# Performance work log

Measured on AMD Instinct MI355X. Metric: run time of the kernel, lower is better.

## Reference

```python
import jax, jax.numpy as jnp
import numpy as np

S_INIT, S_FINAL = 512, 1024
LAYER_DIM, NEXT_DIM, DIM = 512, 512, 1024
BATCH = 32768


def setup_inputs() -> dict:
    rng = np.random.default_rng(0)
    # eigenvector block (trainable 'base') and its 0/1 mask
    base = np.zeros((DIM, DIM), dtype=np.float32)
    base[S_INIT:S_FINAL, S_INIT - LAYER_DIM:S_INIT] = rng.uniform(
        -0.2, 0.2, (NEXT_DIM, LAYER_DIM)).astype(np.float32)
    base_mask = np.zeros((DIM, DIM), dtype=np.float32)
    base_mask[S_INIT:S_FINAL, S_INIT - LAYER_DIM:S_INIT] = 1.0
    eye = np.eye(DIM, dtype=np.float32)
    # eigenvalue diagonal block; NOTE: trainable_diag_mask holds the *random values*
    # (not 0/1), exactly as in the original TF code.
    masks = np.zeros((DIM, DIM), dtype=np.float32)
    masks[S_INIT:S_FINAL, S_INIT:S_FINAL] = np.diag(
        rng.uniform(-1.8, 1.8, NEXT_DIM).astype(np.float32))
    untrainable_diag = eye - masks
    trainable_diag = masks.copy()
    trainable_diag_mask = masks.copy()
    # column masks selecting pass-through rows vs. activated block rows
    mask1 = np.ones((DIM, 1), dtype=np.float32)
    mask1[S_INIT:S_FINAL] = 0.0
    mask2 = np.zeros((DIM, 1), dtype=np.float32)
    mask2[S_INIT:S_FINAL] = 1.0

    key = jax.random.key(0)
    data = jax.random.normal(key, (BATCH, DIM), dtype=jnp.float32)
    return {
        "data": data,
        "base": jnp.asarray(base),
        "base_mask": jnp.asarray(base_mask),
        "eye": jnp.asarray(eye),
        "trainable_diag": jnp.asarray(trainable_diag),
        "trainable_diag_mask": jnp.asarray(trainable_diag_mask),
        "untrainable_diag": jnp.asarray(untrainable_diag),
        "mask1": jnp.asarray(mask1),
        "mask2": jnp.asarray(mask2),
    }


def reference(data, base, base_mask, eye, trainable_diag, trainable_diag_mask,
              untrainable_diag, mask1, mask2):
    # layer = masked base + I ; diag = masked trainable diag + (I - fixed diag)
    layer = base * base_mask + eye                                  # [D, D]
    diag = trainable_diag * trainable_diag_mask + untrainable_diag  # [D, D]
    x = jnp.matmul(2.0 * eye - layer, data.T)                       # [D, B]
    x = jnp.matmul(diag, x)                                         # [D, B]
    x = jnp.matmul(layer, x)                                        # [D, B]
    temp = jax.nn.relu(x)  # relu is elementwise; transpose pair cancels
    x = x * mask1 + temp * mask2                                    # [D, B]
    return x.T                                                      # [B, D]
```

## Files before the change

### kernel.cpp

```cpp
#include <hip/hip_runtime.h>


typedef float f32x4 __attribute__((ext_vector_type(4)));
typedef int   i32x4 __attribute__((ext_vector_type(4)));

#define DIMW   1024
#define HALFD  512
#define BM     64
#define LDAP   520
#define NITER  16

__device__ __forceinline__ unsigned short f2bf(float x) {
    union { float f; unsigned int i; } c;
    c.f = x;
    unsigned int r = c.i + 0x7FFFu + ((c.i >> 16) & 1u);
    return (unsigned short)(r >> 16);
}
__device__ __forceinline__ unsigned int pack2(float a, float b) {
    return (unsigned int)f2bf(a) | ((unsigned int)f2bf(b) << 16);
}

__device__ __forceinline__ void mfma_16x16x32_bf16(f32x4& d, const i32x4& a, const i32x4& b) {
    asm volatile("v_mfma_f32_16x16x32_bf16 %0, %1, %2, %0"
                 : "+v"(d)
                 : "v"(a), "v"(b));
}
__device__ __forceinline__ void acc_fence(f32x4& d) {
    asm volatile("s_nop 7\n\ts_nop 7" : "+v"(d));
}

__global__ __launch_bounds__(512, 4) void spectral_kernel(
    const float* __restrict__ data,
    const float* __restrict__ wsrc,
    const float* __restrict__ td,
    const float* __restrict__ tdm,
    const float* __restrict__ ud,
    float* __restrict__ out)
{
    __shared__ unsigned short As[BM * LDAP];

    const int tid    = (int)threadIdx.x;
    const int lane   = tid & 63;
    const int wn     = tid >> 6;
    const int lane16 = lane & 15;
    const int quad   = lane >> 4;
    const int rowBase = (int)blockIdx.x * BM;

    #pragma unroll
    for (int p = 0; p < 16; ++p) {
        int c  = p * 512 + tid;
        int r  = c >> 7;
        int cc = c & 127;
        size_t off = (size_t)(rowBase + r) * DIMW + cc * 4;
        float4 v = *(const float4*)(data + off);
        *(float4*)(out + off) = v;
        uint2 uu;
        uu.x = pack2(v.x, v.y);
        uu.y = pack2(v.z, v.w);
        *(uint2*)(As + r * LDAP + cc * 4) = uu;
    }

    i32x4 b0[4], b1[4];

    auto LDW = [&](int it, i32x4 (&b)[4]) {
        #pragma unroll
        for (int ni = 0; ni < 4; ++ni) {
            int col = wn * 64 + ni * 16 + lane16;
            const float* p = wsrc + (size_t)(HALFD + col) * DIMW + it * 32 + quad * 8;
            float4 f0 = *(const float4*)p;
            float4 f1 = *(const float4*)(p + 4);
            i32x4 t;
            t[0] = (int)pack2(f0.x, f0.y);  t[1] = (int)pack2(f0.z, f0.w);
            t[2] = (int)pack2(f1.x, f1.y);  t[3] = (int)pack2(f1.z, f1.w);
            b[ni] = t;
        }
    };

    LDW(0, b0);
    LDW(1, b1);
    __syncthreads();

    f32x4 acc[4][4];
    #pragma unroll
    for (int mi = 0; mi < 4; ++mi)
        #pragma unroll
        for (int ni = 0; ni < 4; ++ni)
            acc[mi][ni] = (f32x4){0.f, 0.f, 0.f, 0.f};

    auto STEP = [&](int it, i32x4 (&b)[4]) {
        i32x4 a[4];
        #pragma unroll
        for (int mi = 0; mi < 4; ++mi)
            a[mi] = *(const i32x4*)(As + (mi * 16 + lane16) * LDAP + it * 32 + quad * 8);
        #pragma unroll
        for (int mi = 0; mi < 4; ++mi)
            #pragma unroll
            for (int ni = 0; ni < 4; ++ni)
                mfma_16x16x32_bf16(acc[mi][ni], a[mi], b[ni]);
    };

    #pragma unroll
    for (int it = 0; it < NITER; it += 2) {
        STEP(it, b0);
        if (it + 2 < NITER) LDW(it + 2, b0);
        STEP(it + 1, b1);
        if (it + 3 < NITER) LDW(it + 3, b1);
    }

    #pragma unroll
    for (int mi = 0; mi < 4; ++mi)
        #pragma unroll
        for (int ni = 0; ni < 4; ++ni)
            acc_fence(acc[mi][ni]);

    #pragma unroll
    for (int ni = 0; ni < 4; ++ni) {
        const int nloc = wn * 64 + ni * 16 + lane16;
        const int j  = HALFD + nloc;
        const size_t fi = (size_t)j * DIMW + j;
        const float dv = td[fi] * tdm[fi] + ud[fi];
        #pragma unroll
        for (int mi = 0; mi < 4; ++mi) {
            const int mBase = rowBase + mi * 16 + quad * 4;
            #pragma unroll
            for (int r = 0; r < 4; ++r) {
                const size_t gi = (size_t)(mBase + r) * DIMW + j;
                const float u1 = data[gi];
                const float v  = dv * u1 + (1.0f - dv) * acc[mi][ni][r];
                out[gi] = fmaxf(v, 0.0f);
            }
        }
    }
}

extern "C" void kernel_launch(void* const* d_in, const int* in_sizes, int n_in,
                              void* d_out, int out_size, void* d_ws, size_t ws_size,
                              hipStream_t stream) {
    const float* data = (const float*)d_in[0];
    const float* base = (const float*)d_in[1];
    const float* td   = (const float*)d_in[4];
    const float* tdm  = (const float*)d_in[5];
    const float* ud   = (const float*)d_in[6];
    float* out = (float*)d_out;

    dim3 block(512, 1, 1);
    dim3 grid(32768 / BM, 1, 1);
    spectral_kernel<<<grid, block, 0, stream>>>(data, base, td, tdm, ud, out);
}
```

Before: 367.4 us.

## Split passthrough copy into dedicated blocks and vectorize epilogue via swapped MFMA operands

Adds 256 extra blocks that only copy the pass-through half of the output (the first 512 columns), so GEMM blocks no longer write it. GEMM blocks now load only the left half for the bf16 A tile, batch eight loads before their stores, and cache the diagonal values in shared memory. MFMA operands are swapped so each lane owns four consecutive columns, which lets the epilogue read data and write out with float4 accesses instead of scalar strided ones. The costs are a larger grid with mixed block roles and the copy blocks' tail behaviour.

Result: faster. 346.8 us (-5.6%).

```diff
diff --git a/kernel.cpp b/kernel.cpp
--- a/kernel.cpp
+++ b/kernel.cpp
@@ -9,6 +9,7 @@
 #define BM     64
 #define LDAP   520
 #define NITER  16
+#define NCOPY  256
 
 __device__ __forceinline__ unsigned short f2bf(float x) {
     union { float f; unsigned int i; } c;
@@ -37,27 +38,68 @@
     const float* __restrict__ ud,
     float* __restrict__ out)
 {
+    const int tid = (int)threadIdx.x;
+
+    if ((int)blockIdx.x < NCOPY) {
+        const int rowBase = (int)blockIdx.x * 128;
+        const float4* src = (const float4*)data;
+        float4*       dst = (float4*)out;
+        #pragma unroll
+        for (int h = 0; h < 4; ++h) {
+            float4 v[8];
+            #pragma unroll
+            for (int p = 0; p < 8; ++p) {
+                int c  = (h * 8 + p) * 512 + tid;
+                int r  = c >> 7;
+                int cc = c & 127;
+                v[p] = src[(size_t)(rowBase + r) * (DIMW / 4) + cc];
+            }
+            #pragma unroll
+            for (int p = 0; p < 8; ++p) {
+                int c  = (h * 8 + p) * 512 + tid;
+                int r  = c >> 7;
+                int cc = c & 127;
+                dst[(size_t)(rowBase + r) * (DIMW / 4) + cc] = v[p];
+            }
+        }
+        return;
+    }
+
     __shared__ unsigned short As[BM * LDAP];
+    __shared__ float dsh[HALFD];
 
-    const int tid    = (int)threadIdx.x;
     const int lane   = tid & 63;
     const int wn     = tid >> 6;
     const int lane16 = lane & 15;
     const int quad   = lane >> 4;
-    const int rowBase = (int)blockIdx.x * BM;
+    const int rowBase = ((int)blockIdx.x - NCOPY) * BM;
+
+    {
+        int j = HALFD + tid;
+        size_t fi = (size_t)j * DIMW + j;
+        dsh[tid] = td[fi] * tdm[fi] + ud[fi];
+    }
 
     #pragma unroll
-    for (int p = 0; p < 16; ++p) {
-        int c  = p * 512 + tid;
-        int r  = c >> 7;
-        int cc = c & 127;
-        size_t off = (size_t)(rowBase + r) * DIMW + cc * 4;
-        float4 v = *(const float4*)(data + off);
-        *(float4*)(out + off) = v;
-        uint2 uu;
-        uu.x = pack2(v.x, v.y);
-        uu.y = pack2(v.z, v.w);
-        *(uint2*)(As + r * LDAP + cc * 4) = uu;
+    for (int h = 0; h < 2; ++h) {
+        float4 v[8];
+        #pragma unroll
+        for (int p = 0; p < 8; ++p) {
+            int c  = (h * 8 + p) * 512 + tid;
+            int r  = c >> 7;
+            int cc = c & 127;
+            v[p] = *(const float4*)(data + (size_t)(rowBase + r) * DIMW + cc * 4);
+        }
+        #pragma unroll
+        for (int p = 0; p < 8; ++p) {
+            int c  = (h * 8 + p) * 512 + tid;
+            int r  = c >> 7;
+            int cc = c & 127;
+            uint2 uu;
+            uu.x = pack2(v[p].x, v[p].y);
+            uu.y = pack2(v[p].z, v[p].w);
+            *(uint2*)(As + r * LDAP + cc * 4) = uu;
+        }
     }
 
     i32x4 b0[4], b1[4];
@@ -96,7 +138,7 @@
         for (int mi = 0; mi < 4; ++mi)
             #pragma unroll
             for (int ni = 0; ni < 4; ++ni)
-                mfma_16x16x32_bf16(acc[mi][ni], a[mi], b[ni]);
+                mfma_16x16x32_bf16(acc[mi][ni], b[ni], a[mi]);
     };
 
     #pragma unroll
@@ -114,21 +156,21 @@
             acc_fence(acc[mi][ni]);
 
     #pragma unroll
-    for (int ni = 0; ni < 4; ++ni) {
-        const int nloc = wn * 64 + ni * 16 + lane16;
-        const int j  = HALFD + nloc;
-        const size_t fi = (size_t)j * DIMW + j;
-        const float dv = td[fi] * tdm[fi] + ud[fi];
+    for (int mi = 0; mi < 4; ++mi) {
+        const int row = rowBase + mi * 16 + lane16;
+        const float* drow = data + (size_t)row * DIMW + HALFD;
+        float*       orow = out  + (size_t)row * DIMW + HALFD;
         #pragma unroll
-        for (int mi = 0; mi < 4; ++mi) {
-            const int mBase = rowBase + mi * 16 + quad * 4;
-            #pragma unroll
-            for (int r = 0; r < 4; ++r) {
-                const size_t gi = (size_t)(mBase + r) * DIMW + j;
-                const float u1 = data[gi];
-                const float v  = dv * u1 + (1.0f - dv) * acc[mi][ni][r];
-                out[gi] = fmaxf(v, 0.0f);
-            }
+        for (int ni = 0; ni < 4; ++ni) {
+            const int colb = wn * 64 + ni * 16 + quad * 4;
+            float4 u1 = *(const float4*)(drow + colb);
+            float4 d4 = *(const float4*)(dsh + colb);
+            float4 o;
+            o.x = fmaxf(d4.x * u1.x + (1.0f - d4.x) * acc[mi][ni][0], 0.0f);
+            o.y = fmaxf(d4.y * u1.y + (1.0f - d4.y) * acc[mi][ni][1], 0.0f);
+            o.z = fmaxf(d4.z * u1.z + (1.0f - d4.z) * acc[mi][ni][2], 0.0f);
+            o.w = fmaxf(d4.w * u1.w + (1.0f - d4.w) * acc[mi][ni][3], 0.0f);
+            *(float4*)(orow + colb) = o;
         }
     }
 }
@@ -144,6 +186,6 @@
     float* out = (float*)d_out;
 
     dim3 block(512, 1, 1);
-    dim3 grid(32768 / BM, 1, 1);
+    dim3 grid(NCOPY + 32768 / BM, 1, 1);
     spectral_kernel<<<grid, block, 0, stream>>>(data, base, td, tdm, ud, out);
 }
```
